# Optimization experiments

Measured on AMD Instinct MI355X. Metric: run time of the kernel, lower is better.

The kernel has to match this reference:

```python
import jax, jax.numpy as jnp
import numpy as np

D_MODEL = 1024
NUM_HEADS = 16
HEAD_DIM = D_MODEL // NUM_HEADS


def setup_inputs() -> dict:
    key = jax.random.key(0)
    k_x, k_wqkv, k_bqkv, k_wo, k_bo = jax.random.split(key, 5)
    bound_qkv = 1.0 / np.sqrt(D_MODEL)
    x = jax.random.normal(k_x, (2, 2048, D_MODEL), dtype=jnp.float32)
    # torch nn.Linear init: U(-1/sqrt(fan_in), 1/sqrt(fan_in))
    W_qkv = jax.random.uniform(k_wqkv, (D_MODEL, 3 * D_MODEL), jnp.float32, -bound_qkv, bound_qkv)
    b_qkv = jax.random.uniform(k_bqkv, (3 * D_MODEL,), jnp.float32, -bound_qkv, bound_qkv)
    W_out = jax.random.uniform(k_wo, (D_MODEL, D_MODEL), jnp.float32, -bound_qkv, bound_qkv)
    b_out = jax.random.uniform(k_bo, (D_MODEL,), jnp.float32, -bound_qkv, bound_qkv)
    return {"x": x, "W_qkv": W_qkv, "b_qkv": b_qkv, "W_out": W_out, "b_out": b_out}


def reference(x, W_qkv, b_qkv, W_out, b_out):
    B, T, C = x.shape
    H, Dh = NUM_HEADS, HEAD_DIM
    qkv = x @ W_qkv + b_qkv                      # [B,T,3C]
    q, k, v = jnp.split(qkv, 3, axis=-1)
    # [B,T,C] -> [B,H,T,Dh]
    def to_heads(t):
        return t.reshape(B, T, H, Dh).transpose(0, 2, 1, 3)
    q, k, v = to_heads(q), to_heads(k), to_heads(v)
    scale = 1.0 / np.sqrt(Dh).astype(np.float32)
    scores = jnp.einsum("bhqd,bhkd->bhqk", q, k) * scale   # [B,H,T,T]
    weights = jax.nn.softmax(scores, axis=-1)
    attn = jnp.einsum("bhqk,bhkd->bhqd", weights, v)        # [B,H,T,Dh]
    attn = attn.transpose(0, 2, 1, 3).reshape(B, T, C)
    return attn @ W_out + b_out
```

## Files before the change

### kernel.cpp

```cpp
#include <hip/hip_runtime.h>

typedef __bf16 bf16x8 __attribute__((ext_vector_type(8)));
typedef float f32x4 __attribute__((ext_vector_type(4)));

#define MFMA16(a, b, c) __builtin_amdgcn_mfma_f32_16x16x32_bf16(a, b, c, 0, 0, 0)
#define GLDS16(g, l)                                                              \
  __builtin_amdgcn_global_load_lds((const __attribute__((address_space(1))) void*)(g), \
                                   (__attribute__((address_space(3))) void*)(l), 16, 0, 0)

__global__ __launch_bounds__(256) void cvt_bf16_kernel(const float* __restrict__ in,
                                                       __bf16* __restrict__ out, int n4) {
  int i = blockIdx.x * 256 + threadIdx.x;
  if (i < n4) {
    float4 v = ((const float4*)in)[i];
    union { __bf16 b[4]; uint2 u; } t;
    t.b[0] = (__bf16)v.x; t.b[1] = (__bf16)v.y;
    t.b[2] = (__bf16)v.z; t.b[3] = (__bf16)v.w;
    ((uint2*)out)[i] = t.u;
  }
}

__global__ __launch_bounds__(256) void transpose_w_kernel(const float* __restrict__ Wq,
                                                          __bf16* __restrict__ WqT,
                                                          const float* __restrict__ Wo,
                                                          __bf16* __restrict__ WoT) {
  const int Kd = 1024;
  int bx = blockIdx.x;
  const float* W; __bf16* WT; int Nd, n0;
  if (bx < 96) { W = Wq; WT = WqT; Nd = 3072; n0 = bx * 32; }
  else         { W = Wo; WT = WoT; Nd = 1024; n0 = (bx - 96) * 32; }
  __shared__ float tile[32][33];
  int k0 = blockIdx.y * 32;
  int tid = threadIdx.x;
  int kk = tid >> 3, nn = (tid & 7) * 4;
  float4 v = *(const float4*)&W[(size_t)(k0 + kk) * Nd + n0 + nn];
  tile[kk][nn] = v.x; tile[kk][nn + 1] = v.y;
  tile[kk][nn + 2] = v.z; tile[kk][nn + 3] = v.w;
  __syncthreads();
  int n2 = tid >> 3, k2 = (tid & 7) * 4;
  union { __bf16 b[4]; uint2 u; } t;
  t.b[0] = (__bf16)tile[k2][n2];
  t.b[1] = (__bf16)tile[k2 + 1][n2];
  t.b[2] = (__bf16)tile[k2 + 2][n2];
  t.b[3] = (__bf16)tile[k2 + 3][n2];
  *(uint2*)&WT[(size_t)(n0 + n2) * Kd + k0 + k2] = t.u;
}

template <bool OUT_F32, int NT>
__global__ __launch_bounds__(256) void gemm_kernel(const __bf16* __restrict__ A,
                                                   const __bf16* __restrict__ BT,
                                                   const float* __restrict__ bias,
                                                   void* __restrict__ Cout, int N,
                                                   int qn, float qs) {
  const int K = 1024;
  const int NJ = NT / 32;
  __shared__ __align__(16) __bf16 As[128 * 32];
  __shared__ __align__(16) __bf16 Bs[NT * 32];
  int tid = threadIdx.x;
  int wave = tid >> 6, lane = tid & 63;
  int quad = lane >> 4, l16 = lane & 15;
  int m0 = blockIdx.x * 128, n0 = blockIdx.y * NT;
  int wm = (wave >> 1) * 64, wn = (wave & 1) * (NT / 2);

  int srow = tid >> 2, scol = (tid & 3) * 8;
  const __bf16* aptr = A + (size_t)(m0 + srow) * K + scol;
  const __bf16* bptr = BT + (size_t)(n0 + srow) * K + scol;
  __bf16* asl = &As[(size_t)wave * 512];
  __bf16* bsl = &Bs[(size_t)wave * 512];

  f32x4 acc[4][NJ] = {};
  for (int k0 = 0; k0 < K; k0 += 32) {
    GLDS16(aptr + k0, asl);
    GLDS16(aptr + (size_t)64 * K + k0, asl + 2048);
    GLDS16(bptr + k0, bsl);
    if (NT == 128) GLDS16(bptr + (size_t)64 * K + k0, bsl + 2048);
    __syncthreads();
    bf16x8 af[4], bf[NJ];
    for (int i = 0; i < 4; i++)
      af[i] = *(bf16x8*)&As[(wm + i * 16 + l16) * 32 + quad * 8];
    for (int j = 0; j < NJ; j++)
      bf[j] = *(bf16x8*)&Bs[(wn + j * 16 + l16) * 32 + quad * 8];
    for (int i = 0; i < 4; i++)
      for (int j = 0; j < NJ; j++)
        acc[i][j] = MFMA16(af[i], bf[j], acc[i][j]);
    __syncthreads();
  }
  for (int j = 0; j < NJ; j++) {
    int col = n0 + wn + j * 16 + l16;
    float bv = bias[col];
    float sc = (col < qn) ? qs : 1.0f;
    for (int i = 0; i < 4; i++) {
      int rowb = m0 + wm + i * 16 + quad * 4;
      for (int r = 0; r < 4; r++) {
        float v = (acc[i][j][r] + bv) * sc;
        if (OUT_F32)
          ((float*)Cout)[(size_t)(rowb + r) * N + col] = v;
        else
          ((__bf16*)Cout)[(size_t)(rowb + r) * N + col] = (__bf16)v;
      }
    }
  }
}

__global__ __launch_bounds__(256) void transpose_v_kernel(const __bf16* __restrict__ qkv,
                                                          __bf16* __restrict__ Vt) {
  const int T = 2048, C3 = 3072;
  __shared__ __align__(16) __bf16 tile[64][72];
  int t0 = blockIdx.x * 64;
  int h = blockIdx.y, b = blockIdx.z;
  int tid = threadIdx.x;
  int tt = tid >> 2, c = (tid & 3) * 16;
  const __bf16* src = qkv + (size_t)(b * T + t0 + tt) * C3 + 2048 + h * 64 + c;
  *(uint4*)&tile[tt][c] = *(const uint4*)src;
  *(uint4*)&tile[tt][c + 8] = *(const uint4*)(src + 8);
  __syncthreads();
  int dd = tid >> 2, t2 = (tid & 3) * 16;
  union { __bf16 b_[16]; uint4 u[2]; } o;
  for (int i = 0; i < 16; i++) o.b_[i] = tile[t2 + i][dd];
  __bf16* dst = Vt + ((size_t)(b * 16 + h) * 64 + dd) * T + t0 + t2;
  *(uint4*)dst = o.u[0];
  *(uint4*)(dst + 8) = o.u[1];
}

__global__ __launch_bounds__(256) void attn_kernel(const __bf16* __restrict__ qkv,
                                                   const __bf16* __restrict__ Vt,
                                                   __bf16* __restrict__ O) {
  const int T = 2048, C3 = 3072;
  int q0 = blockIdx.x * 64;
  int h = blockIdx.y, b = blockIdx.z;
  int tid = threadIdx.x, wave = tid >> 6, lane = tid & 63;
  int quad = lane >> 4, l16 = lane & 15;

  __shared__ __align__(16) __bf16 Ks[64 * 64];
  __shared__ __align__(16) __bf16 Vts[64 * 64];
  __shared__ __align__(16) __bf16 Ps[4][16 * 72];

  const __bf16* qp = qkv + (size_t)(b * T + q0 + wave * 16 + l16) * C3 + h * 64;
  bf16x8 aq0 = *(const bf16x8*)(qp + quad * 8);
  bf16x8 aq1 = *(const bf16x8*)(qp + 32 + quad * 8);

  const __bf16* kbase = qkv + (size_t)(b * T) * C3 + 1024 + h * 64;
  const __bf16* vbase = Vt + (size_t)(b * 16 + h) * 64 * T;

  int srow = lane >> 3;
  int scol = ((lane & 7) ^ srow) * 8;
  int r0 = wave * 16 + srow;
  __bf16* kdst0 = &Ks[(size_t)(wave * 16) * 64];
  __bf16* kdst1 = &Ks[(size_t)(wave * 16 + 8) * 64];
  __bf16* vdst0 = &Vts[(size_t)(wave * 16) * 64];
  __bf16* vdst1 = &Vts[(size_t)(wave * 16 + 8) * 64];

  int xb0 = ((quad ^ (l16 & 7)) * 8);
  int xb1 = (((4 + quad) ^ (l16 & 7)) * 8);

  f32x4 o[4] = {};
  f32x4 lacc = {};
  bf16x8 ones;
  for (int i = 0; i < 8; i++) ones[i] = (__bf16)1.0f;

  for (int t0 = 0; t0 < T; t0 += 64) {
    __syncthreads();
    GLDS16(kbase + (size_t)(t0 + r0) * C3 + scol, kdst0);
    GLDS16(kbase + (size_t)(t0 + r0 + 8) * C3 + scol, kdst1);
    GLDS16(vbase + (size_t)r0 * T + t0 + scol, vdst0);
    GLDS16(vbase + (size_t)(r0 + 8) * T + t0 + scol, vdst1);
    __syncthreads();

    f32x4 s[4] = {};
    for (int ct = 0; ct < 4; ct++) {
      int row = ct * 16 + l16;
      bf16x8 bk0 = *(bf16x8*)&Ks[row * 64 + xb0];
      bf16x8 bk1 = *(bf16x8*)&Ks[row * 64 + xb1];
      s[ct] = MFMA16(aq0, bk0, s[ct]);
      s[ct] = MFMA16(aq1, bk1, s[ct]);
    }

    for (int ct = 0; ct < 4; ct++) {
      int cp = (((ct * 2 + (l16 >> 3)) ^ quad) << 3) | (l16 & 7);
      for (int r = 0; r < 4; r++) {
        float p = __builtin_amdgcn_exp2f(s[ct][r]);
        Ps[wave][(quad * 4 + r) * 72 + cp] = (__bf16)p;
      }
    }

    for (int kc = 0; kc < 2; kc++) {
      int cpb = (((kc * 4 + quad) ^ (l16 >> 2)) << 3);
      bf16x8 ap = *(bf16x8*)&Ps[wave][l16 * 72 + cpb];
      lacc = MFMA16(ap, ones, lacc);
      int xv = kc ? xb1 : xb0;
      for (int nt = 0; nt < 4; nt++) {
        bf16x8 bv = *(bf16x8*)&Vts[(nt * 16 + l16) * 64 + xv];
        o[nt] = MFMA16(ap, bv, o[nt]);
      }
    }
  }

  f32x4 inv;
  for (int r = 0; r < 4; r++) inv[r] = 1.0f / lacc[r];
  for (int nt = 0; nt < 4; nt++)
    for (int r = 0; r < 4; r++) {
      int row = q0 + wave * 16 + quad * 4 + r;
      O[(size_t)(b * T + row) * 1024 + h * 64 + nt * 16 + l16] =
          (__bf16)(o[nt][r] * inv[r]);
    }
}

extern "C" void kernel_launch(void* const* d_in, const int* in_sizes, int n_in,
                              void* d_out, int out_size, void* d_ws, size_t ws_size,
                              hipStream_t stream) {
  const float* x = (const float*)d_in[0];
  const float* W_qkv = (const float*)d_in[1];
  const float* b_qkv = (const float*)d_in[2];
  const float* W_out = (const float*)d_in[3];
  const float* b_out = (const float*)d_in[4];
  float* out = (float*)d_out;

  char* ws = (char*)d_ws;
  __bf16* WqkvT = (__bf16*)(ws);
  __bf16* WoT = (__bf16*)(ws + 6291456);
  __bf16* xb = (__bf16*)(ws + 8388608);
  __bf16* qkvb = (__bf16*)(ws + 16777216);
  __bf16* Vt = (__bf16*)(ws + 41943040);
  __bf16* attnb = xb;

  const float cs = 0.125f * 1.44269504089f;

  cvt_bf16_kernel<<<4096, 256, 0, stream>>>(x, xb, 1048576);
  transpose_w_kernel<<<dim3(128, 32), 256, 0, stream>>>(W_qkv, WqkvT, W_out, WoT);
  gemm_kernel<false, 128><<<dim3(32, 24), 256, 0, stream>>>(xb, WqkvT, b_qkv, qkvb, 3072,
                                                            1024, cs);
  transpose_v_kernel<<<dim3(32, 16, 2), 256, 0, stream>>>(qkvb, Vt);
  attn_kernel<<<dim3(32, 16, 2), 256, 0, stream>>>(qkvb, Vt, attnb);
  gemm_kernel<true, 64><<<dim3(32, 16), 256, 0, stream>>>(attnb, WoT, b_out, out, 1024,
                                                          0, 1.0f);
}
```

Measured before the change: 203.1 us.

## Rewrite attention kernel with 32x32 MFMA, double-buffered K/V, and two-wave blocks

Rewrites the attention kernel so each of two waves handles 32 query rows using 32x32x16 bf16 MFMAs instead of four waves using 16x16x32. K and V tiles are double-buffered in LDS with async global-to-LDS loads for the next tile issued before computing the current one, and wave 0 loads K while wave 1 loads V. The goal is more work per MFMA, fewer LDS reads per FLOP, and overlap of memory with compute. In exchange, blocks shrink to 128 threads, accumulator register pressure rises, and the LDS layouts and swizzles are new.

```diff
diff --git a/kernel.cpp b/kernel.cpp
--- a/kernel.cpp
+++ b/kernel.cpp
@@ -2,8 +2,10 @@
 
 typedef __bf16 bf16x8 __attribute__((ext_vector_type(8)));
 typedef float f32x4 __attribute__((ext_vector_type(4)));
+typedef float f32x16 __attribute__((ext_vector_type(16)));
 
 #define MFMA16(a, b, c) __builtin_amdgcn_mfma_f32_16x16x32_bf16(a, b, c, 0, 0, 0)
+#define MFMA32(a, b, c) __builtin_amdgcn_mfma_f32_32x32x16_bf16(a, b, c, 0, 0, 0)
 #define GLDS16(g, l)                                                              \
   __builtin_amdgcn_global_load_lds((const __attribute__((address_space(1))) void*)(g), \
                                    (__attribute__((address_space(3))) void*)(l), 16, 0, 0)
@@ -122,87 +124,100 @@
   *(uint4*)(dst + 8) = o.u[1];
 }
 
-__global__ __launch_bounds__(256) void attn_kernel(const __bf16* __restrict__ qkv,
+__global__ __launch_bounds__(128) void attn_kernel(const __bf16* __restrict__ qkv,
                                                    const __bf16* __restrict__ Vt,
                                                    __bf16* __restrict__ O) {
   const int T = 2048, C3 = 3072;
   int q0 = blockIdx.x * 64;
   int h = blockIdx.y, b = blockIdx.z;
   int tid = threadIdx.x, wave = tid >> 6, lane = tid & 63;
-  int quad = lane >> 4, l16 = lane & 15;
-
-  __shared__ __align__(16) __bf16 Ks[64 * 64];
-  __shared__ __align__(16) __bf16 Vts[64 * 64];
-  __shared__ __align__(16) __bf16 Ps[4][16 * 72];
-
-  const __bf16* qp = qkv + (size_t)(b * T + q0 + wave * 16 + l16) * C3 + h * 64;
-  bf16x8 aq0 = *(const bf16x8*)(qp + quad * 8);
-  bf16x8 aq1 = *(const bf16x8*)(qp + 32 + quad * 8);
+  int l31 = lane & 31, hw = lane >> 5;
+
+  __shared__ __align__(16) __bf16 KV[2][8192];
+  __shared__ __align__(16) __bf16 Ps[2][2048];
+
+  const __bf16* qp = qkv + (size_t)(b * T + q0 + wave * 32 + l31) * C3 + h * 64 + hw * 8;
+  bf16x8 aq[4];
+  for (int c = 0; c < 4; c++) aq[c] = *(const bf16x8*)(qp + c * 16);
 
   const __bf16* kbase = qkv + (size_t)(b * T) * C3 + 1024 + h * 64;
   const __bf16* vbase = Vt + (size_t)(b * 16 + h) * 64 * T;
 
-  int srow = lane >> 3;
-  int scol = ((lane & 7) ^ srow) * 8;
-  int r0 = wave * 16 + srow;
-  __bf16* kdst0 = &Ks[(size_t)(wave * 16) * 64];
-  __bf16* kdst1 = &Ks[(size_t)(wave * 16 + 8) * 64];
-  __bf16* vdst0 = &Vts[(size_t)(wave * 16) * 64];
-  __bf16* vdst1 = &Vts[(size_t)(wave * 16 + 8) * 64];
-
-  int xb0 = ((quad ^ (l16 & 7)) * 8);
-  int xb1 = (((4 + quad) ^ (l16 & 7)) * 8);
-
-  f32x4 o[4] = {};
-  f32x4 lacc = {};
+  const __bf16* ksrc = kbase + (size_t)l31 * C3 + hw * 8;
+  const __bf16* vsrc = vbase + (size_t)l31 * T + hw * 8;
+
+  int kchi = (lane >> 4) & 1, rh = (lane >> 3) & 1, jj = lane & 7;
+  int wbase = kchi * 512 + rh * 256 + (hw ^ rh) * 32 + jj;
+  int rbase = hw * 256 + (l31 ^ (hw * 4)) * 8;
+
+  f32x16 o0 = {}, o1 = {}, ls = {};
   bf16x8 ones;
   for (int i = 0; i < 8; i++) ones[i] = (__bf16)1.0f;
 
+  if (wave == 0) {
+    for (int ct = 0; ct < 2; ct++)
+      for (int c = 0; c < 4; c++)
+        GLDS16(ksrc + (size_t)ct * 32 * C3 + c * 16, &KV[0][(ct * 4 + c) * 512]);
+  } else {
+    for (int kc = 0; kc < 4; kc++)
+      for (int dt = 0; dt < 2; dt++)
+        GLDS16(vsrc + (size_t)dt * 32 * T + kc * 16, &KV[0][4096 + (kc * 2 + dt) * 512]);
+  }
+
   for (int t0 = 0; t0 < T; t0 += 64) {
+    int buf = (t0 >> 6) & 1;
     __syncthreads();
-    GLDS16(kbase + (size_t)(t0 + r0) * C3 + scol, kdst0);
-    GLDS16(kbase + (size_t)(t0 + r0 + 8) * C3 + scol, kdst1);
-    GLDS16(vbase + (size_t)r0 * T + t0 + scol, vdst0);
-    GLDS16(vbase + (size_t)(r0 + 8) * T + t0 + scol, vdst1);
-    __syncthreads();
-
-    f32x4 s[4] = {};
-    for (int ct = 0; ct < 4; ct++) {
-      int row = ct * 16 + l16;
-      bf16x8 bk0 = *(bf16x8*)&Ks[row * 64 + xb0];
-      bf16x8 bk1 = *(bf16x8*)&Ks[row * 64 + xb1];
-      s[ct] = MFMA16(aq0, bk0, s[ct]);
-      s[ct] = MFMA16(aq1, bk1, s[ct]);
-    }
-
-    for (int ct = 0; ct < 4; ct++) {
-      int cp = (((ct * 2 + (l16 >> 3)) ^ quad) << 3) | (l16 & 7);
-      for (int r = 0; r < 4; r++) {
-        float p = __builtin_amdgcn_exp2f(s[ct][r]);
-        Ps[wave][(quad * 4 + r) * 72 + cp] = (__bf16)p;
-      }
-    }
-
-    for (int kc = 0; kc < 2; kc++) {
-      int cpb = (((kc * 4 + quad) ^ (l16 >> 2)) << 3);
-      bf16x8 ap = *(bf16x8*)&Ps[wave][l16 * 72 + cpb];
-      lacc = MFMA16(ap, ones, lacc);
-      int xv = kc ? xb1 : xb0;
-      for (int nt = 0; nt < 4; nt++) {
-        bf16x8 bv = *(bf16x8*)&Vts[(nt * 16 + l16) * 64 + xv];
-        o[nt] = MFMA16(ap, bv, o[nt]);
-      }
-    }
-  }
-
-  f32x4 inv;
-  for (int r = 0; r < 4; r++) inv[r] = 1.0f / lacc[r];
-  for (int nt = 0; nt < 4; nt++)
-    for (int r = 0; r < 4; r++) {
-      int row = q0 + wave * 16 + quad * 4 + r;
-      O[(size_t)(b * T + row) * 1024 + h * 64 + nt * 16 + l16] =
-          (__bf16)(o[nt][r] * inv[r]);
-    }
+
+    if (t0 + 64 < T) {
+      if (wave == 0) {
+        const __bf16* ks = ksrc + (size_t)(t0 + 64) * C3;
+        for (int ct = 0; ct < 2; ct++)
+          for (int c = 0; c < 4; c++)
+            GLDS16(ks + (size_t)ct * 32 * C3 + c * 16, &KV[buf ^ 1][(ct * 4 + c) * 512]);
+      } else {
+        const __bf16* vs = vsrc + t0 + 64;
+        for (int kc = 0; kc < 4; kc++)
+          for (int dt = 0; dt < 2; dt++)
+            GLDS16(vs + (size_t)dt * 32 * T + kc * 16,
+                   &KV[buf ^ 1][4096 + (kc * 2 + dt) * 512]);
+      }
+    }
+
+    const __bf16* Kb = &KV[buf][0];
+    const __bf16* Vb = &KV[buf][4096];
+
+    for (int ct = 0; ct < 2; ct++) {
+      f32x16 ss = {};
+      for (int c = 0; c < 4; c++) {
+        bf16x8 bk = *(const bf16x8*)&Kb[(ct * 4 + c) * 512 + lane * 8];
+        ss = MFMA32(aq[c], bk, ss);
+      }
+#pragma unroll
+      for (int reg = 0; reg < 16; reg++) {
+        int dq = (reg & 3) + 8 * (reg >> 2);
+        float p = __builtin_amdgcn_exp2f(ss[reg]);
+        Ps[wave][wbase + ct * 1024 + dq * 8] = (__bf16)p;
+      }
+    }
+
+    for (int kc = 0; kc < 4; kc++) {
+      bf16x8 ap = *(const bf16x8*)&Ps[wave][rbase + kc * 512];
+      ls = MFMA32(ap, ones, ls);
+      bf16x8 bv0 = *(const bf16x8*)&Vb[(kc * 2 + 0) * 512 + lane * 8];
+      bf16x8 bv1 = *(const bf16x8*)&Vb[(kc * 2 + 1) * 512 + lane * 8];
+      o0 = MFMA32(ap, bv0, o0);
+      o1 = MFMA32(ap, bv1, o1);
+    }
+  }
+
+  __bf16* obase = O + (size_t)(b * T + q0 + wave * 32 + 4 * hw) * 1024 + h * 64 + l31;
+#pragma unroll
+  for (int reg = 0; reg < 16; reg++) {
+    int dq = (reg & 3) + 8 * (reg >> 2);
+    float inv = 1.0f / ls[reg];
+    obase[(size_t)dq * 1024] = (__bf16)(o0[reg] * inv);
+    obase[(size_t)dq * 1024 + 32] = (__bf16)(o1[reg] * inv);
+  }
 }
 
 extern "C" void kernel_launch(void* const* d_in, const int* in_sizes, int n_in,
@@ -230,7 +245,7 @@
   gemm_kernel<false, 128><<<dim3(32, 24), 256, 0, stream>>>(xb, WqkvT, b_qkv, qkvb, 3072,
                                                             1024, cs);
   transpose_v_kernel<<<dim3(32, 16, 2), 256, 0, stream>>>(qkvb, Vt);
-  attn_kernel<<<dim3(32, 16, 2), 256, 0, stream>>>(qkvb, Vt, attnb);
+  attn_kernel<<<dim3(32, 16, 2), 128, 0, stream>>>(qkvb, Vt, attnb);
   gemm_kernel<true, 64><<<dim3(32, 16), 256, 0, stream>>>(attnb, WoT, b_out, out, 1024,
                                                           0, 1.0f);
 }
```

Measured after the change: 209.8 us. 3.3% more time.
